# Kernel optimization log

Measured on AMD Instinct MI355X. Metric: run time of the kernel, lower is better.

The kernel has to match this reference:

```python
import jax, jax.numpy as jnp
import numpy as np

M, K, N = 8192, 4096, 4096  # tokens, in_features, out_features

def setup_inputs() -> dict:
    key = jax.random.key(0)
    k1, k2, k3 = jax.random.split(key, 3)
    x = jax.random.normal(k1, (M, K), dtype=jnp.float32)
    # kaiming_uniform_(a=sqrt(5)) on [out,in] -> uniform(-1/sqrt(in), 1/sqrt(in))
    bound = 1.0 / np.sqrt(K)
    weight = jax.random.uniform(k2, (N, K), dtype=jnp.float32, minval=-bound, maxval=bound)
    bias = jax.random.uniform(k3, (N,), dtype=jnp.float32, minval=-bound, maxval=bound)
    return {
        "x": x,
        "weight": weight,
        "bias": bias,
        "input_scale": jnp.float32(1.0),
        "weight_scale": jnp.float32(1.0),
    }


def reference(x, weight, bias, input_scale, weight_scale):
    # Quantize input and weight to fp8 e4m3 (per-tensor scale = 1.0 in module),
    # then dequant-matmul: out = (x_fp8 @ w_fp8^T) * scale_a * scale_b + bias,
    # matching torch._scaled_mm semantics with out_dtype=float32.
    x_fp8 = x.astype(jnp.float8_e4m3fn)
    w_fp8 = weight.astype(jnp.float8_e4m3fn)
    out = jnp.einsum(
        "mk,nk->mn",
        x_fp8.astype(jnp.float32),
        w_fp8.astype(jnp.float32),
    ) * (input_scale * weight_scale)
    return out + bias[None, :]
```

## Files before the change

kernel.cpp:

```cpp
#include <hip/hip_runtime.h>
#include <hip/hip_fp8.h>
#include <cstdint>

typedef float f32x4 __attribute__((ext_vector_type(4)));
typedef int i32x8 __attribute__((ext_vector_type(8)));
typedef long long i64;

static constexpr int Mdim = 8192;
static constexpr int Kdim = 4096;
static constexpr int Ndim = 4096;

static constexpr int BM = 256, BN = 256, BK = 128;
static constexpr int NT = Kdim / BK;
static constexpr int NWG_M = Mdim / BM;
static constexpr int NWG_N = Ndim / BN;
static constexpr int NWG = NWG_M * NWG_N;
static_assert(NT >= 4, "pipeline needs >=4 K-tiles");

__device__ __forceinline__ uint8_t f32_to_e4m3(float f) {
  return (uint8_t)__hip_cvt_float_to_fp8(f, __HIP_SATFINITE, __HIP_E4M3);
}

__global__ __launch_bounds__(256) void quant_fp8_kernel(
    const float* __restrict__ in, uint8_t* __restrict__ out, int n_vec16) {
  const int stride = gridDim.x * blockDim.x;
  for (int i = blockIdx.x * blockDim.x + threadIdx.x; i < n_vec16; i += stride) {
    const float4* src = reinterpret_cast<const float4*>(in) + (size_t)i * 4;
    float4 f0 = src[0], f1 = src[1], f2 = src[2], f3 = src[3];
    const float v[16] = {f0.x, f0.y, f0.z, f0.w, f1.x, f1.y, f1.z, f1.w,
                         f2.x, f2.y, f2.z, f2.w, f3.x, f3.y, f3.z, f3.w};
    union alignas(16) {
      uint32_t u[4];
      uint8_t b[16];
    } r;
#pragma unroll
    for (int j = 0; j < 16; ++j) r.b[j] = f32_to_e4m3(v[j]);
    reinterpret_cast<uint4*>(out)[i] = *reinterpret_cast<const uint4*>(r.u);
  }
}

__device__ __forceinline__ void gload_lds16(const uint8_t* g, uint8_t* l) {
  __builtin_amdgcn_global_load_lds(
      (const __attribute__((address_space(1))) void*)g,
      (__attribute__((address_space(3))) void*)l, 16, 0, 0);
}

__device__ __forceinline__ f32x4 mx_mfma(i32x8 a, i32x8 b, f32x4 c) {
  return __builtin_amdgcn_mfma_scale_f32_16x16x128_f8f6f4(
      a, b, c, 0, 0, 0, 0x7f7f7f7f, 0, 0x7f7f7f7f);
}

__global__ __launch_bounds__(512, 2) void gemm_fp8_mx_256(
    const uint8_t* __restrict__ Aq, const uint8_t* __restrict__ Bq,
    const float* __restrict__ bias, const float* __restrict__ sa,
    const float* __restrict__ sb, float* __restrict__ C) {
  __shared__ alignas(16) uint8_t sA[2][BM * BK];
  __shared__ alignas(16) uint8_t sB[2][BN * BK];

  int wg = (int)blockIdx.x;
  wg = (wg & 7) * (NWG / 8) + (wg >> 3);
  const int bm0 = (wg / NWG_N) * BM;
  const int bn0 = (wg % NWG_N) * BN;

  const int t = (int)threadIdx.x;
  const int lane = t & 63;
  const int wave = t >> 6;
  const int wm = wave >> 2;
  const int wn = wave & 3;

  const int srow = t >> 3;
  const int sc16 = (t & 7) ^ (srow & 7);
  const uint8_t* aBase = Aq + (size_t)(bm0 + srow) * Kdim + sc16 * 16;
  const uint8_t* bBase = Bq + (size_t)(bn0 + srow) * Kdim + sc16 * 16;
  const int ldsOff = t * 16;

  auto stage = [&](int buf, int kt) {
    const int kb = kt * BK;
#pragma unroll
    for (int i = 0; i < 4; ++i)
      gload_lds16(aBase + kb + (size_t)i * (64 * Kdim),
                  &sA[buf][i * 8192 + ldsOff]);
#pragma unroll
    for (int i = 0; i < 4; ++i)
      gload_lds16(bBase + kb + (size_t)i * (64 * Kdim),
                  &sB[buf][i * 8192 + ldsOff]);
  };

  const int r7 = lane & 7;
  const int kg = (lane >> 4) * 2;
  const int off0 = (kg ^ r7) * 16;
  const int off1 = ((kg + 1) ^ r7) * 16;
  const int rbA = (wm * 128 + (lane & 15)) * BK;
  const int rbB = (wn * 64 + (lane & 15)) * BK;

  auto ldfrag = [&](const uint8_t* base) -> i32x8 {
    union {
      i32x8 v;
      int4 h[2];
    } u;
    u.h[0] = *reinterpret_cast<const int4*>(base + off0);
    u.h[1] = *reinterpret_cast<const int4*>(base + off1);
    return u.v;
  };

  f32x4 acc[8][4] = {};

  stage(0, 0);
  stage(1, 1);
  asm volatile("s_waitcnt vmcnt(8)" ::: "memory");
  __builtin_amdgcn_s_barrier();
  asm volatile("" ::: "memory");

#pragma unroll 1
  for (int kt = 0; kt < NT; ++kt) {
    const int c = kt & 1;
    const uint8_t* A = &sA[c][0];
    const uint8_t* B = &sB[c][0];

    i32x8 bf[4];
#pragma unroll
    for (int n = 0; n < 4; ++n) bf[n] = ldfrag(B + rbB + n * 16 * BK);
    i32x8 a0 = ldfrag(A + rbA + 0 * 16 * BK);
    i32x8 a1 = ldfrag(A + rbA + 1 * 16 * BK);
    __builtin_amdgcn_s_setprio(1);
#pragma unroll
    for (int n = 0; n < 4; ++n) acc[0][n] = mx_mfma(a0, bf[n], acc[0][n]);
#pragma unroll
    for (int n = 0; n < 4; ++n) acc[1][n] = mx_mfma(a1, bf[n], acc[1][n]);
    __builtin_amdgcn_s_setprio(0);

    a0 = ldfrag(A + rbA + 2 * 16 * BK);
    a1 = ldfrag(A + rbA + 3 * 16 * BK);
    __builtin_amdgcn_s_setprio(1);
#pragma unroll
    for (int n = 0; n < 4; ++n) acc[2][n] = mx_mfma(a0, bf[n], acc[2][n]);
#pragma unroll
    for (int n = 0; n < 4; ++n) acc[3][n] = mx_mfma(a1, bf[n], acc[3][n]);
    __builtin_amdgcn_s_setprio(0);

    a0 = ldfrag(A + rbA + 4 * 16 * BK);
    a1 = ldfrag(A + rbA + 5 * 16 * BK);
    __builtin_amdgcn_s_setprio(1);
#pragma unroll
    for (int n = 0; n < 4; ++n) acc[4][n] = mx_mfma(a0, bf[n], acc[4][n]);
#pragma unroll
    for (int n = 0; n < 4; ++n) acc[5][n] = mx_mfma(a1, bf[n], acc[5][n]);
    __builtin_amdgcn_s_setprio(0);

    a0 = ldfrag(A + rbA + 6 * 16 * BK);
    a1 = ldfrag(A + rbA + 7 * 16 * BK);
    asm volatile("s_waitcnt lgkmcnt(0)" ::: "memory");
    __builtin_amdgcn_s_barrier();
    asm volatile("" ::: "memory");
    if (kt + 2 < NT) stage(c, kt + 2);
    __builtin_amdgcn_s_setprio(1);
#pragma unroll
    for (int n = 0; n < 4; ++n) acc[6][n] = mx_mfma(a0, bf[n], acc[6][n]);
#pragma unroll
    for (int n = 0; n < 4; ++n) acc[7][n] = mx_mfma(a1, bf[n], acc[7][n]);
    __builtin_amdgcn_s_setprio(0);

    if (kt + 2 < NT) {
      asm volatile("s_waitcnt vmcnt(8)" ::: "memory");
      __builtin_amdgcn_s_barrier();
      asm volatile("" ::: "memory");
    } else if (kt + 1 < NT) {
      asm volatile("s_waitcnt vmcnt(0)" ::: "memory");
      __builtin_amdgcn_s_barrier();
      asm volatile("" ::: "memory");
    }
  }

  const float scale = sa[0] * sb[0];
  const int orow0 = bm0 + wm * 128 + ((lane >> 4) << 2);
  const int ocol0 = bn0 + wn * 64 + (lane & 15);
#pragma unroll
  for (int n = 0; n < 4; ++n) {
    const int col = ocol0 + n * 16;
    const float bv = bias[col];
#pragma unroll
    for (int m = 0; m < 8; ++m) {
      const int row = orow0 + m * 16;
#pragma unroll
      for (int r = 0; r < 4; ++r)
        C[(size_t)(row + r) * Ndim + col] = acc[m][n][r] * scale + bv;
    }
  }
}

__device__ __forceinline__ void stage16_cvt(const float* g, uint8_t* l) {
  const float4* s = reinterpret_cast<const float4*>(g);
  float4 f0 = s[0], f1 = s[1], f2 = s[2], f3 = s[3];
  const float v[16] = {f0.x, f0.y, f0.z, f0.w, f1.x, f1.y, f1.z, f1.w,
                       f2.x, f2.y, f2.z, f2.w, f3.x, f3.y, f3.z, f3.w};
  union alignas(16) {
    uint32_t u[4];
    uint8_t b[16];
  } r;
#pragma unroll
  for (int j = 0; j < 16; ++j) r.b[j] = f32_to_e4m3(v[j]);
  *reinterpret_cast<uint4*>(l) = *reinterpret_cast<const uint4*>(r.u);
}

__global__ __launch_bounds__(256) void gemm_fp8_fused_kernel(
    const float* __restrict__ X, const float* __restrict__ W,
    const float* __restrict__ bias, const float* __restrict__ sa,
    const float* __restrict__ sb, float* __restrict__ C) {
  constexpr int FBM = 128, FBN = 128, FBK = 64;
  constexpr int FNWG_N = Ndim / FBN;
  __shared__ alignas(16) uint8_t As[FBM * FBK];
  __shared__ alignas(16) uint8_t Bs[FBN * FBK];

  int wg = (int)blockIdx.x;
  const int nwg = (Mdim / FBM) * FNWG_N;
  wg = (wg & 7) * (nwg / 8) + (wg >> 3);
  const int bm0 = (wg / FNWG_N) * FBM;
  const int bn0 = (wg % FNWG_N) * FBN;

  const int t = (int)threadIdx.x;
  const int lane = t & 63;
  const int wave = t >> 6;
  const int wm = wave >> 1, wn = wave & 1;

  const int c0 = t, c1 = t + 256;
  const int r0 = c0 >> 2, col0 = (c0 & 3) * 16;
  const int r1 = c1 >> 2, col1 = (c1 & 3) * 16;
  const float* xa0 = X + (size_t)(bm0 + r0) * Kdim + col0;
  const float* xa1 = X + (size_t)(bm0 + r1) * Kdim + col1;
  const float* wb0 = W + (size_t)(bn0 + r0) * Kdim + col0;
  const float* wb1 = W + (size_t)(bn0 + r1) * Kdim + col1;

  const int arow = (wm * 64 + (lane & 15)) * FBK;
  const int brow = (wn * 64 + (lane & 15)) * FBK;
  const int koff = (lane >> 4) * 8;

  f32x4 acc[4][4] = {};

  for (int kt = 0; kt < Kdim / FBK; ++kt) {
    const int kb = kt * FBK;
    stage16_cvt(xa0 + kb, As + c0 * 16);
    stage16_cvt(xa1 + kb, As + c1 * 16);
    stage16_cvt(wb0 + kb, Bs + c0 * 16);
    stage16_cvt(wb1 + kb, Bs + c1 * 16);
    __syncthreads();
#pragma unroll
    for (int kk = 0; kk < FBK / 32; ++kk) {
      i64 a[4], b[4];
#pragma unroll
      for (int m = 0; m < 4; ++m)
        a[m] = *reinterpret_cast<const i64*>(&As[arow + m * 16 * FBK + kk * 32 + koff]);
#pragma unroll
      for (int n = 0; n < 4; ++n)
        b[n] = *reinterpret_cast<const i64*>(&Bs[brow + n * 16 * FBK + kk * 32 + koff]);
#pragma unroll
      for (int m = 0; m < 4; ++m)
#pragma unroll
        for (int n = 0; n < 4; ++n)
          acc[m][n] = __builtin_amdgcn_mfma_f32_16x16x32_fp8_fp8(
              a[m], b[n], acc[m][n], 0, 0, 0);
    }
    __syncthreads();
  }

  const float scale = sa[0] * sb[0];
  const int orow0 = bm0 + wm * 64 + ((lane >> 4) << 2);
  const int ocol0 = bn0 + wn * 64 + (lane & 15);
#pragma unroll
  for (int n = 0; n < 4; ++n) {
    const int col = ocol0 + n * 16;
    const float bv = bias[col];
#pragma unroll
    for (int m = 0; m < 4; ++m) {
      const int row = orow0 + m * 16;
#pragma unroll
      for (int r = 0; r < 4; ++r)
        C[(size_t)(row + r) * Ndim + col] = acc[m][n][r] * scale + bv;
    }
  }
}

extern "C" void kernel_launch(void* const* d_in, const int* in_sizes, int n_in,
                              void* d_out, int out_size, void* d_ws, size_t ws_size,
                              hipStream_t stream) {
  const float* x = (const float*)d_in[0];
  const float* w = (const float*)d_in[1];
  const float* bias = (const float*)d_in[2];
  const float* s_in = (const float*)d_in[3];
  const float* s_w = (const float*)d_in[4];
  float* out = (float*)d_out;

  const size_t needA = (size_t)Mdim * Kdim;
  const size_t needB = (size_t)Ndim * Kdim;

  if (ws_size >= needA + needB) {
    uint8_t* Aq = (uint8_t*)d_ws;
    uint8_t* Bq = Aq + needA;
    quant_fp8_kernel<<<2048, 256, 0, stream>>>(x, Aq, (int)(needA / 16));
    quant_fp8_kernel<<<2048, 256, 0, stream>>>(w, Bq, (int)(needB / 16));
    gemm_fp8_mx_256<<<NWG, 512, 0, stream>>>(Aq, Bq, bias, s_in, s_w, out);
  } else {
    gemm_fp8_fused_kernel<<<(Mdim / 128) * (Ndim / 128), 256, 0, stream>>>(
        x, w, bias, s_in, s_w, out);
  }
}
```

Before: 196.9 us.

## Split tile staging into interleaved half-loads with per-phase barriers

Splits the global-to-LDS staging of A and B tiles into four half-tile loads issued between the four MFMA phases. A is prefetched one tile ahead into the alternate buffer and B two tiles ahead. Each phase is fenced with workgroup barriers and sched_barriers so loads and MFMAs interleave more evenly across waves. This spreads memory traffic across the iteration but adds several barriers per K-step, which can stall waves.

```diff
diff --git a/kernel.cpp b/kernel.cpp
--- a/kernel.cpp
+++ b/kernel.cpp
@@ -74,16 +74,19 @@
   const uint8_t* bBase = Bq + (size_t)(bn0 + srow) * Kdim + sc16 * 16;
   const int ldsOff = t * 16;
 
-  auto stage = [&](int buf, int kt) {
-    const int kb = kt * BK;
-#pragma unroll
-    for (int i = 0; i < 4; ++i)
-      gload_lds16(aBase + kb + (size_t)i * (64 * Kdim),
-                  &sA[buf][i * 8192 + ldsOff]);
-#pragma unroll
-    for (int i = 0; i < 4; ++i)
-      gload_lds16(bBase + kb + (size_t)i * (64 * Kdim),
-                  &sB[buf][i * 8192 + ldsOff]);
+  auto stageA = [&](int buf, int kt, int h) {
+    const size_t kb = (size_t)kt * BK;
+#pragma unroll
+    for (int i = 0; i < 2; ++i)
+      gload_lds16(aBase + kb + (size_t)(h * 128 + i * 64) * Kdim,
+                  &sA[buf][h * 16384 + i * 8192 + ldsOff]);
+  };
+  auto stageB = [&](int buf, int kt, int h) {
+    const size_t kb = (size_t)kt * BK;
+#pragma unroll
+    for (int i = 0; i < 2; ++i)
+      gload_lds16(bBase + kb + (size_t)(h * 128 + i * 64) * Kdim,
+                  &sB[buf][h * 16384 + i * 8192 + ldsOff]);
   };
 
   const int r7 = lane & 7;
@@ -105,15 +108,20 @@
 
   f32x4 acc[8][4] = {};
 
-  stage(0, 0);
-  stage(1, 1);
-  asm volatile("s_waitcnt vmcnt(8)" ::: "memory");
+  stageA(0, 0, 0);
+  stageA(0, 0, 1);
+  stageB(0, 0, 0);
+  stageB(0, 0, 1);
+  stageB(1, 1, 0);
+  stageB(1, 1, 1);
+  asm volatile("s_waitcnt vmcnt(4)" ::: "memory");
   __builtin_amdgcn_s_barrier();
-  asm volatile("" ::: "memory");
+  __builtin_amdgcn_sched_barrier(0);
 
 #pragma unroll 1
   for (int kt = 0; kt < NT; ++kt) {
     const int c = kt & 1;
+    const int cn = c ^ 1;
     const uint8_t* A = &sA[c][0];
     const uint8_t* B = &sB[c][0];
 
@@ -122,53 +130,68 @@
     for (int n = 0; n < 4; ++n) bf[n] = ldfrag(B + rbB + n * 16 * BK);
     i32x8 a0 = ldfrag(A + rbA + 0 * 16 * BK);
     i32x8 a1 = ldfrag(A + rbA + 1 * 16 * BK);
+    if (kt + 1 < NT) stageA(cn, kt + 1, 0);
+    __builtin_amdgcn_s_barrier();
+    asm volatile("s_waitcnt lgkmcnt(0)" ::: "memory");
+    __builtin_amdgcn_sched_barrier(0);
     __builtin_amdgcn_s_setprio(1);
 #pragma unroll
     for (int n = 0; n < 4; ++n) acc[0][n] = mx_mfma(a0, bf[n], acc[0][n]);
 #pragma unroll
     for (int n = 0; n < 4; ++n) acc[1][n] = mx_mfma(a1, bf[n], acc[1][n]);
     __builtin_amdgcn_s_setprio(0);
+    __builtin_amdgcn_s_barrier();
+    __builtin_amdgcn_sched_barrier(0);
 
     a0 = ldfrag(A + rbA + 2 * 16 * BK);
     a1 = ldfrag(A + rbA + 3 * 16 * BK);
+    if (kt + 1 < NT) stageA(cn, kt + 1, 1);
+    __builtin_amdgcn_s_barrier();
+    asm volatile("s_waitcnt lgkmcnt(0)" ::: "memory");
+    __builtin_amdgcn_sched_barrier(0);
     __builtin_amdgcn_s_setprio(1);
 #pragma unroll
     for (int n = 0; n < 4; ++n) acc[2][n] = mx_mfma(a0, bf[n], acc[2][n]);
 #pragma unroll
     for (int n = 0; n < 4; ++n) acc[3][n] = mx_mfma(a1, bf[n], acc[3][n]);
     __builtin_amdgcn_s_setprio(0);
+    __builtin_amdgcn_s_barrier();
+    __builtin_amdgcn_sched_barrier(0);
 
     a0 = ldfrag(A + rbA + 4 * 16 * BK);
     a1 = ldfrag(A + rbA + 5 * 16 * BK);
+    if (kt + 2 < NT) stageB(c, kt + 2, 0);
+    __builtin_amdgcn_s_barrier();
+    asm volatile("s_waitcnt lgkmcnt(0)" ::: "memory");
+    __builtin_amdgcn_sched_barrier(0);
     __builtin_amdgcn_s_setprio(1);
 #pragma unroll
     for (int n = 0; n < 4; ++n) acc[4][n] = mx_mfma(a0, bf[n], acc[4][n]);
 #pragma unroll
     for (int n = 0; n < 4; ++n) acc[5][n] = mx_mfma(a1, bf[n], acc[5][n]);
     __builtin_amdgcn_s_setprio(0);
+    __builtin_amdgcn_s_barrier();
+    __builtin_amdgcn_sched_barrier(0);
 
     a0 = ldfrag(A + rbA + 6 * 16 * BK);
     a1 = ldfrag(A + rbA + 7 * 16 * BK);
+    if (kt + 2 < NT) stageB(c, kt + 2, 1);
+    __builtin_amdgcn_s_barrier();
     asm volatile("s_waitcnt lgkmcnt(0)" ::: "memory");
-    __builtin_amdgcn_s_barrier();
-    asm volatile("" ::: "memory");
-    if (kt + 2 < NT) stage(c, kt + 2);
+    __builtin_amdgcn_sched_barrier(0);
     __builtin_amdgcn_s_setprio(1);
 #pragma unroll
     for (int n = 0; n < 4; ++n) acc[6][n] = mx_mfma(a0, bf[n], acc[6][n]);
 #pragma unroll
     for (int n = 0; n < 4; ++n) acc[7][n] = mx_mfma(a1, bf[n], acc[7][n]);
     __builtin_amdgcn_s_setprio(0);
-
     if (kt + 2 < NT) {
-      asm volatile("s_waitcnt vmcnt(8)" ::: "memory");
-      __builtin_amdgcn_s_barrier();
-      asm volatile("" ::: "memory");
-    } else if (kt + 1 < NT) {
+      asm volatile("s_waitcnt vmcnt(4)" ::: "memory");
+    } else {
       asm volatile("s_waitcnt vmcnt(0)" ::: "memory");
-      __builtin_amdgcn_s_barrier();
-      asm volatile("" ::: "memory");
     }
+    __builtin_amdgcn_s_barrier();
+    __builtin_amdgcn_sched_barrier(0);
   }
 
   const float scale = sa[0] * sb[0];
```

Result: slower. 202.7 us (+2.9%).

## Split A/B staging with asymmetric prefetch depths and reordered LDS fragment loads

Applied to the files above, without the earlier changes.

Splits the global-to-LDS staging into separate A and B loaders, so A is prefetched one tile ahead and B two tiles ahead. A's next tile is issued at the top of each iteration, and B's refill is issued after a mid-iteration barrier. More A fragments are loaded up front, and sched_barrier fences pin the order of LDS reads and MFMAs. The intent is to spread global loads across the iteration and overlap LDS reads with MFMA work. The cost is higher register pressure, an extra barrier per iteration, and a shallower prefetch for A that may expose memory latency.

```diff
diff --git a/kernel.cpp b/kernel.cpp
--- a/kernel.cpp
+++ b/kernel.cpp
@@ -74,15 +74,18 @@
   const uint8_t* bBase = Bq + (size_t)(bn0 + srow) * Kdim + sc16 * 16;
   const int ldsOff = t * 16;
 
-  auto stage = [&](int buf, int kt) {
-    const int kb = kt * BK;
+  auto stageA = [&](int buf, int kt) {
+    const size_t kb = (size_t)kt * BK;
 #pragma unroll
     for (int i = 0; i < 4; ++i)
-      gload_lds16(aBase + kb + (size_t)i * (64 * Kdim),
+      gload_lds16(aBase + kb + (size_t)(i * 64) * Kdim,
                   &sA[buf][i * 8192 + ldsOff]);
+  };
+  auto stageB = [&](int buf, int kt) {
+    const size_t kb = (size_t)kt * BK;
 #pragma unroll
     for (int i = 0; i < 4; ++i)
-      gload_lds16(bBase + kb + (size_t)i * (64 * Kdim),
+      gload_lds16(bBase + kb + (size_t)(i * 64) * Kdim,
                   &sB[buf][i * 8192 + ldsOff]);
   };
 
@@ -105,70 +108,95 @@
 
   f32x4 acc[8][4] = {};
 
-  stage(0, 0);
-  stage(1, 1);
-  asm volatile("s_waitcnt vmcnt(8)" ::: "memory");
+  stageA(0, 0);
+  stageB(0, 0);
+  stageB(1, 1);
+  asm volatile("s_waitcnt vmcnt(4)" ::: "memory");
   __builtin_amdgcn_s_barrier();
-  asm volatile("" ::: "memory");
+  __builtin_amdgcn_sched_barrier(0);
 
 #pragma unroll 1
   for (int kt = 0; kt < NT; ++kt) {
     const int c = kt & 1;
+    const int cn = c ^ 1;
     const uint8_t* A = &sA[c][0];
     const uint8_t* B = &sB[c][0];
 
-    i32x8 bf[4];
-#pragma unroll
-    for (int n = 0; n < 4; ++n) bf[n] = ldfrag(B + rbB + n * 16 * BK);
+    if (kt + 1 < NT) stageA(cn, kt + 1);
+
+    i32x8 bf0 = ldfrag(B + rbB + 0 * 16 * BK);
+    i32x8 bf1 = ldfrag(B + rbB + 1 * 16 * BK);
+    i32x8 bf2 = ldfrag(B + rbB + 2 * 16 * BK);
+    i32x8 bf3 = ldfrag(B + rbB + 3 * 16 * BK);
     i32x8 a0 = ldfrag(A + rbA + 0 * 16 * BK);
     i32x8 a1 = ldfrag(A + rbA + 1 * 16 * BK);
+    i32x8 a2 = ldfrag(A + rbA + 2 * 16 * BK);
+    i32x8 a3 = ldfrag(A + rbA + 3 * 16 * BK);
+    __builtin_amdgcn_sched_barrier(0);
+
     __builtin_amdgcn_s_setprio(1);
-#pragma unroll
-    for (int n = 0; n < 4; ++n) acc[0][n] = mx_mfma(a0, bf[n], acc[0][n]);
-#pragma unroll
-    for (int n = 0; n < 4; ++n) acc[1][n] = mx_mfma(a1, bf[n], acc[1][n]);
+    acc[0][0] = mx_mfma(a0, bf0, acc[0][0]);
+    acc[0][1] = mx_mfma(a0, bf1, acc[0][1]);
+    acc[0][2] = mx_mfma(a0, bf2, acc[0][2]);
+    acc[0][3] = mx_mfma(a0, bf3, acc[0][3]);
+    acc[1][0] = mx_mfma(a1, bf0, acc[1][0]);
+    acc[1][1] = mx_mfma(a1, bf1, acc[1][1]);
+    acc[1][2] = mx_mfma(a1, bf2, acc[1][2]);
+    acc[1][3] = mx_mfma(a1, bf3, acc[1][3]);
     __builtin_amdgcn_s_setprio(0);
 
-    a0 = ldfrag(A + rbA + 2 * 16 * BK);
-    a1 = ldfrag(A + rbA + 3 * 16 * BK);
+    __builtin_amdgcn_s_barrier();
+    if (kt + 2 < NT) stageB(c, kt + 2);
+    __builtin_amdgcn_sched_barrier(0);
+
+    i32x8 a4 = ldfrag(A + rbA + 4 * 16 * BK);
+    i32x8 a5 = ldfrag(A + rbA + 5 * 16 * BK);
+    __builtin_amdgcn_sched_barrier(0);
+
     __builtin_amdgcn_s_setprio(1);
-#pragma unroll
-    for (int n = 0; n < 4; ++n) acc[2][n] = mx_mfma(a0, bf[n], acc[2][n]);
-#pragma unroll
-    for (int n = 0; n < 4; ++n) acc[3][n] = mx_mfma(a1, bf[n], acc[3][n]);
+    acc[2][0] = mx_mfma(a2, bf0, acc[2][0]);
+    acc[2][1] = mx_mfma(a2, bf1, acc[2][1]);
+    acc[2][2] = mx_mfma(a2, bf2, acc[2][2]);
+    acc[2][3] = mx_mfma(a2, bf3, acc[2][3]);
+    acc[3][0] = mx_mfma(a3, bf0, acc[3][0]);
+    acc[3][1] = mx_mfma(a3, bf1, acc[3][1]);
+    acc[3][2] = mx_mfma(a3, bf2, acc[3][2]);
+    acc[3][3] = mx_mfma(a3, bf3, acc[3][3]);
     __builtin_amdgcn_s_setprio(0);
 
-    a0 = ldfrag(A + rbA + 4 * 16 * BK);
-    a1 = ldfrag(A + rbA + 5 * 16 * BK);
+    i32x8 a6 = ldfrag(A + rbA + 6 * 16 * BK);
+    i32x8 a7 = ldfrag(A + rbA + 7 * 16 * BK);
+    __builtin_amdgcn_sched_barrier(0);
+
     __builtin_amdgcn_s_setprio(1);
-#pragma unroll
-    for (int n = 0; n < 4; ++n) acc[4][n] = mx_mfma(a0, bf[n], acc[4][n]);
-#pragma unroll
-    for (int n = 0; n < 4; ++n) acc[5][n] = mx_mfma(a1, bf[n], acc[5][n]);
+    acc[4][0] = mx_mfma(a4, bf0, acc[4][0]);
+    acc[4][1] = mx_mfma(a4, bf1, acc[4][1]);
+    acc[4][2] = mx_mfma(a4, bf2, acc[4][2]);
+    acc[4][3] = mx_mfma(a4, bf3, acc[4][3]);
+    acc[5][0] = mx_mfma(a5, bf0, acc[5][0]);
+    acc[5][1] = mx_mfma(a5, bf1, acc[5][1]);
+    acc[5][2] = mx_mfma(a5, bf2, acc[5][2]);
+    acc[5][3] = mx_mfma(a5, bf3, acc[5][3]);
     __builtin_amdgcn_s_setprio(0);
 
-    a0 = ldfrag(A + rbA + 6 * 16 * BK);
-    a1 = ldfrag(A + rbA + 7 * 16 * BK);
-    asm volatile("s_waitcnt lgkmcnt(0)" ::: "memory");
+    __builtin_amdgcn_s_setprio(1);
+    acc[6][0] = mx_mfma(a6, bf0, acc[6][0]);
+    acc[6][1] = mx_mfma(a6, bf1, acc[6][1]);
+    acc[6][2] = mx_mfma(a6, bf2, acc[6][2]);
+    acc[6][3] = mx_mfma(a6, bf3, acc[6][3]);
+    acc[7][0] = mx_mfma(a7, bf0, acc[7][0]);
+    acc[7][1] = mx_mfma(a7, bf1, acc[7][1]);
+    acc[7][2] = mx_mfma(a7, bf2, acc[7][2]);
+    acc[7][3] = mx_mfma(a7, bf3, acc[7][3]);
+    __builtin_amdgcn_s_setprio(0);
+
+    if (kt + 2 < NT) {
+      asm volatile("s_waitcnt vmcnt(4)" ::: "memory");
+    } else {
+      asm volatile("s_waitcnt vmcnt(0)" ::: "memory");
+    }
     __builtin_amdgcn_s_barrier();
-    asm volatile("" ::: "memory");
-    if (kt + 2 < NT) stage(c, kt + 2);
-    __builtin_amdgcn_s_setprio(1);
-#pragma unroll
-    for (int n = 0; n < 4; ++n) acc[6][n] = mx_mfma(a0, bf[n], acc[6][n]);
-#pragma unroll
-    for (int n = 0; n < 4; ++n) acc[7][n] = mx_mfma(a1, bf[n], acc[7][n]);
-    __builtin_amdgcn_s_setprio(0);
-
-    if (kt + 2 < NT) {
-      asm volatile("s_waitcnt vmcnt(8)" ::: "memory");
-      __builtin_amdgcn_s_barrier();
-      asm volatile("" ::: "memory");
-    } else if (kt + 1 < NT) {
-      asm volatile("s_waitcnt vmcnt(0)" ::: "memory");
-      __builtin_amdgcn_s_barrier();
-      asm volatile("" ::: "memory");
-    }
+    __builtin_amdgcn_sched_barrier(0);
   }
 
   const float scale = sa[0] * sb[0];
```

Result: slower. 201.4 us (+2.3%).

## Use 4-wave workgroups with 128x128 per-wave tiles and simpler double buffering

Applied to the files above, without the earlier changes.

The GEMM moves from 8 waves (each computing 128x64) to 4 waves (each computing 128x128) per 256x256 tile. Each wave now issues 64 MFMAs per K-step, and fragment reuse per wave is higher. The pipeline becomes a plain double buffer that prefetches the next tile before a barrier, replacing the previous staggered two-ahead schedule with priority hints. In exchange, the per-wave accumulator grows to 256 floats, which pushes register pressure near the limit and leaves fewer waves per CU to hide latency.

```diff
diff --git a/kernel.cpp b/kernel.cpp
--- a/kernel.cpp
+++ b/kernel.cpp
@@ -50,7 +50,7 @@
       a, b, c, 0, 0, 0, 0x7f7f7f7f, 0, 0x7f7f7f7f);
 }
 
-__global__ __launch_bounds__(512, 2) void gemm_fp8_mx_256(
+__global__ __launch_bounds__(256, 1) void gemm_fp8_mx_w4(
     const uint8_t* __restrict__ Aq, const uint8_t* __restrict__ Bq,
     const float* __restrict__ bias, const float* __restrict__ sa,
     const float* __restrict__ sb, float* __restrict__ C) {
@@ -65,8 +65,8 @@
   const int t = (int)threadIdx.x;
   const int lane = t & 63;
   const int wave = t >> 6;
-  const int wm = wave >> 2;
-  const int wn = wave & 3;
+  const int wm = wave >> 1;
+  const int wn = wave & 1;
 
   const int srow = t >> 3;
   const int sc16 = (t & 7) ^ (srow & 7);
@@ -74,16 +74,16 @@
   const uint8_t* bBase = Bq + (size_t)(bn0 + srow) * Kdim + sc16 * 16;
   const int ldsOff = t * 16;
 
-  auto stage = [&](int buf, int kt) {
-    const int kb = kt * BK;
-#pragma unroll
-    for (int i = 0; i < 4; ++i)
-      gload_lds16(aBase + kb + (size_t)i * (64 * Kdim),
-                  &sA[buf][i * 8192 + ldsOff]);
-#pragma unroll
-    for (int i = 0; i < 4; ++i)
-      gload_lds16(bBase + kb + (size_t)i * (64 * Kdim),
-                  &sB[buf][i * 8192 + ldsOff]);
+  auto stageAB = [&](int buf, int kt) {
+    const size_t kb = (size_t)kt * BK;
+#pragma unroll
+    for (int i = 0; i < 8; ++i)
+      gload_lds16(aBase + kb + (size_t)(i * 32) * Kdim,
+                  &sA[buf][i * 4096 + ldsOff]);
+#pragma unroll
+    for (int i = 0; i < 8; ++i)
+      gload_lds16(bBase + kb + (size_t)(i * 32) * Kdim,
+                  &sB[buf][i * 4096 + ldsOff]);
   };
 
   const int r7 = lane & 7;
@@ -91,7 +91,7 @@
   const int off0 = (kg ^ r7) * 16;
   const int off1 = ((kg + 1) ^ r7) * 16;
   const int rbA = (wm * 128 + (lane & 15)) * BK;
-  const int rbB = (wn * 64 + (lane & 15)) * BK;
+  const int rbB = (wn * 128 + (lane & 15)) * BK;
 
   auto ldfrag = [&](const uint8_t* base) -> i32x8 {
     union {
@@ -103,79 +103,47 @@
     return u.v;
   };
 
-  f32x4 acc[8][4] = {};
-
-  stage(0, 0);
-  stage(1, 1);
-  asm volatile("s_waitcnt vmcnt(8)" ::: "memory");
-  __builtin_amdgcn_s_barrier();
-  asm volatile("" ::: "memory");
+  f32x4 acc[8][8] = {};
+
+  stageAB(0, 0);
 
 #pragma unroll 1
-  for (int kt = 0; kt < NT; ++kt) {
-    const int c = kt & 1;
+  for (int j = 0; j < NT; ++j) {
+    const int c = j & 1;
     const uint8_t* A = &sA[c][0];
     const uint8_t* B = &sB[c][0];
 
-    i32x8 bf[4];
-#pragma unroll
-    for (int n = 0; n < 4; ++n) bf[n] = ldfrag(B + rbB + n * 16 * BK);
-    i32x8 a0 = ldfrag(A + rbA + 0 * 16 * BK);
-    i32x8 a1 = ldfrag(A + rbA + 1 * 16 * BK);
-    __builtin_amdgcn_s_setprio(1);
-#pragma unroll
-    for (int n = 0; n < 4; ++n) acc[0][n] = mx_mfma(a0, bf[n], acc[0][n]);
-#pragma unroll
-    for (int n = 0; n < 4; ++n) acc[1][n] = mx_mfma(a1, bf[n], acc[1][n]);
-    __builtin_amdgcn_s_setprio(0);
-
-    a0 = ldfrag(A + rbA + 2 * 16 * BK);
-    a1 = ldfrag(A + rbA + 3 * 16 * BK);
-    __builtin_amdgcn_s_setprio(1);
-#pragma unroll
-    for (int n = 0; n < 4; ++n) acc[2][n] = mx_mfma(a0, bf[n], acc[2][n]);
-#pragma unroll
-    for (int n = 0; n < 4; ++n) acc[3][n] = mx_mfma(a1, bf[n], acc[3][n]);
-    __builtin_amdgcn_s_setprio(0);
-
-    a0 = ldfrag(A + rbA + 4 * 16 * BK);
-    a1 = ldfrag(A + rbA + 5 * 16 * BK);
-    __builtin_amdgcn_s_setprio(1);
-#pragma unroll
-    for (int n = 0; n < 4; ++n) acc[4][n] = mx_mfma(a0, bf[n], acc[4][n]);
-#pragma unroll
-    for (int n = 0; n < 4; ++n) acc[5][n] = mx_mfma(a1, bf[n], acc[5][n]);
-    __builtin_amdgcn_s_setprio(0);
-
-    a0 = ldfrag(A + rbA + 6 * 16 * BK);
-    a1 = ldfrag(A + rbA + 7 * 16 * BK);
-    asm volatile("s_waitcnt lgkmcnt(0)" ::: "memory");
+    if (j + 1 < NT) {
+      stageAB(c ^ 1, j + 1);
+      asm volatile("s_waitcnt vmcnt(16)" ::: "memory");
+    } else {
+      asm volatile("s_waitcnt vmcnt(0)" ::: "memory");
+    }
     __builtin_amdgcn_s_barrier();
-    asm volatile("" ::: "memory");
-    if (kt + 2 < NT) stage(c, kt + 2);
-    __builtin_amdgcn_s_setprio(1);
-#pragma unroll
-    for (int n = 0; n < 4; ++n) acc[6][n] = mx_mfma(a0, bf[n], acc[6][n]);
-#pragma unroll
-    for (int n = 0; n < 4; ++n) acc[7][n] = mx_mfma(a1, bf[n], acc[7][n]);
-    __builtin_amdgcn_s_setprio(0);
-
-    if (kt + 2 < NT) {
-      asm volatile("s_waitcnt vmcnt(8)" ::: "memory");
-      __builtin_amdgcn_s_barrier();
-      asm volatile("" ::: "memory");
-    } else if (kt + 1 < NT) {
-      asm volatile("s_waitcnt vmcnt(0)" ::: "memory");
-      __builtin_amdgcn_s_barrier();
-      asm volatile("" ::: "memory");
-    }
+    __builtin_amdgcn_sched_barrier(0);
+
+    i32x8 bf[8], af[8];
+#pragma unroll
+    for (int n = 0; n < 8; ++n) bf[n] = ldfrag(B + rbB + n * 16 * BK);
+    af[0] = ldfrag(A + rbA + 0 * 16 * BK);
+    af[1] = ldfrag(A + rbA + 1 * 16 * BK);
+#pragma unroll
+    for (int m = 0; m < 8; ++m) {
+      if (m < 6) af[m + 2] = ldfrag(A + rbA + (m + 2) * 16 * BK);
+#pragma unroll
+      for (int n = 0; n < 8; ++n) acc[m][n] = mx_mfma(af[m], bf[n], acc[m][n]);
+    }
+
+    __builtin_amdgcn_sched_barrier(0);
+    __builtin_amdgcn_s_barrier();
+    __builtin_amdgcn_sched_barrier(0);
   }
 
   const float scale = sa[0] * sb[0];
   const int orow0 = bm0 + wm * 128 + ((lane >> 4) << 2);
-  const int ocol0 = bn0 + wn * 64 + (lane & 15);
-#pragma unroll
-  for (int n = 0; n < 4; ++n) {
+  const int ocol0 = bn0 + wn * 128 + (lane & 15);
+#pragma unroll
+  for (int n = 0; n < 8; ++n) {
     const int col = ocol0 + n * 16;
     const float bv = bias[col];
 #pragma unroll
@@ -297,7 +265,7 @@
     uint8_t* Bq = Aq + needA;
     quant_fp8_kernel<<<2048, 256, 0, stream>>>(x, Aq, (int)(needA / 16));
     quant_fp8_kernel<<<2048, 256, 0, stream>>>(w, Bq, (int)(needB / 16));
-    gemm_fp8_mx_256<<<NWG, 512, 0, stream>>>(Aq, Bq, bias, s_in, s_w, out);
+    gemm_fp8_mx_w4<<<NWG, 256, 0, stream>>>(Aq, Bq, bias, s_in, s_w, out);
   } else {
     gemm_fp8_fused_kernel<<<(Mdim / 128) * (Ndim / 128), 256, 0, stream>>>(
         x, w, bias, s_in, s_w, out);
```

Result: slower. 255.6 us (+29.9%).
